# Performance work log

Measured on AMD Instinct MI355X. Metric: run time of the kernel, lower is better.

The kernel has to match this reference:

```python
import jax, jax.numpy as jnp
import numpy as np

EPS_BN = 1e-5
EPS_LN = 1e-5
B_, CIN, COUT, H_, W_ = 8, 64, 128, 64, 64
DSTATE, DCONV, EXPAND = 16, 4, 2
DINNER = EXPAND * COUT            # 256
DTRANK = (COUT + 15) // 16        # 8


def setup_inputs() -> dict:
    key = jax.random.key(0)
    ks = jax.random.split(key, 24)
    g = lambda i, shape, s=0.02: jax.random.normal(ks[i], shape, jnp.float32) * s
    inp = {}
    inp["x"] = jax.random.normal(ks[0], (B_, CIN, H_, W_), jnp.float32)
    # conv-bn-relu x2
    inp["conv1_w"] = g(1, (COUT, CIN, 3, 3), 0.05)
    inp["conv1_b"] = jnp.zeros((COUT,), jnp.float32)
    inp["bn1_g"] = jnp.ones((COUT,), jnp.float32)
    inp["bn1_b"] = jnp.zeros((COUT,), jnp.float32)
    inp["bn1_m"] = g(2, (COUT,), 0.1)
    inp["bn1_v"] = jnp.ones((COUT,), jnp.float32)
    inp["conv2_w"] = g(3, (COUT, COUT, 3, 3), 0.05)
    inp["conv2_b"] = jnp.zeros((COUT,), jnp.float32)
    inp["bn2_g"] = jnp.ones((COUT,), jnp.float32)
    inp["bn2_b"] = jnp.zeros((COUT,), jnp.float32)
    inp["bn2_m"] = g(4, (COUT,), 0.1)
    inp["bn2_v"] = jnp.ones((COUT,), jnp.float32)
    # Mamba params (mamba_ssm defaults: projections bias-free except dt_proj)
    inp["in_proj_w"] = g(5, (2 * DINNER, COUT))
    inp["conv1d_w"] = g(6, (DINNER, 1, DCONV), 0.1)   # depthwise
    inp["conv1d_b"] = jnp.zeros((DINNER,), jnp.float32)
    inp["x_proj_w"] = g(7, (DTRANK + 2 * DSTATE, DINNER))
    inp["dt_proj_w"] = g(8, (DINNER, DTRANK), 0.1)
    inp["dt_proj_b"] = g(9, (DINNER,), 0.5)
    # S4D-real init: A = -[1..d_state] per channel
    A = jnp.tile(jnp.arange(1, DSTATE + 1, dtype=jnp.float32)[None, :], (DINNER, 1))
    inp["A_log"] = jnp.log(A)
    inp["D"] = jnp.ones((DINNER,), jnp.float32)
    inp["out_proj_w"] = g(10, (COUT, DINNER))
    inp["ln_g"] = jnp.ones((COUT,), jnp.float32)
    inp["ln_b"] = jnp.zeros((COUT,), jnp.float32)
    return inp


def _conv3x3(x, w, b):
    y = jax.lax.conv_general_dilated(x, w, (1, 1), ((1, 1), (1, 1)),
                                     dimension_numbers=("NCHW", "OIHW", "NCHW"))
    return y + b[None, :, None, None]


def _bn_eval(x, g, b, m, v):
    inv = jax.lax.rsqrt(v + EPS_BN)
    return (x - m[None, :, None, None]) * (g * inv)[None, :, None, None] + b[None, :, None, None]


def _mamba(x_flat, in_proj_w, conv1d_w, conv1d_b, x_proj_w, dt_proj_w, dt_proj_b, A_log, D, out_proj_w):
    # x_flat: (B, L, C)
    Bsz, L, _ = x_flat.shape
    xz = jnp.einsum("blc,ec->ble", x_flat, in_proj_w)          # (B, L, 2*di)
    xm, z = jnp.split(xz, 2, axis=-1)                           # each (B, L, di)
    # causal depthwise conv1d over time
    xt = jnp.transpose(xm, (0, 2, 1))                           # (B, di, L)
    xt = jax.lax.conv_general_dilated(xt, conv1d_w, (1,), ((DCONV - 1, 0),),
                                      dimension_numbers=("NCH", "OIH", "NCH"),
                                      feature_group_count=DINNER)
    xt = xt + conv1d_b[None, :, None]
    x_ssm = jax.nn.silu(jnp.transpose(xt, (0, 2, 1)))           # (B, L, di)
    xdb = jnp.einsum("bld,ed->ble", x_ssm, x_proj_w)            # (B, L, dt_rank+2*ds)
    dt_r = xdb[..., :DTRANK]
    Bm = xdb[..., DTRANK:DTRANK + DSTATE]                       # (B, L, ds)
    Cm = xdb[..., DTRANK + DSTATE:]                             # (B, L, ds)
    dt = jax.nn.softplus(jnp.einsum("blr,dr->bld", dt_r, dt_proj_w) + dt_proj_b)
    A = -jnp.exp(A_log)                                         # (di, ds)

    def step(h, inp):
        dt_t, B_t, C_t, x_t = inp                               # (B,di) (B,ds) (B,ds) (B,di)
        dA = jnp.exp(dt_t[:, :, None] * A)                      # (B, di, ds)
        h = dA * h + (dt_t * x_t)[:, :, None] * B_t[:, None, :]
        y = jnp.einsum("bds,bs->bd", h, C_t)
        return h, y

    xs = (jnp.swapaxes(dt, 0, 1), jnp.swapaxes(Bm, 0, 1),
          jnp.swapaxes(Cm, 0, 1), jnp.swapaxes(x_ssm, 0, 1))
    h0 = jnp.zeros((Bsz, DINNER, DSTATE), jnp.float32)
    _, ys = jax.lax.scan(step, h0, xs)                          # (L, B, di)
    y = jnp.swapaxes(ys, 0, 1) + D * x_ssm
    y = y * jax.nn.silu(z)
    return jnp.einsum("bld,od->blo", y, out_proj_w)             # (B, L, C)


def reference(x, conv1_w, conv1_b, bn1_g, bn1_b, bn1_m, bn1_v,
              conv2_w, conv2_b, bn2_g, bn2_b, bn2_m, bn2_v,
              in_proj_w, conv1d_w, conv1d_b, x_proj_w, dt_proj_w, dt_proj_b,
              A_log, D, out_proj_w, ln_g, ln_b):
    h = jax.nn.relu(_bn_eval(_conv3x3(x, conv1_w, conv1_b), bn1_g, bn1_b, bn1_m, bn1_v))
    h = jax.nn.relu(_bn_eval(_conv3x3(h, conv2_w, conv2_b), bn2_g, bn2_b, bn2_m, bn2_v))
    Bsz, C, Hh, Ww = h.shape
    seq = jnp.transpose(h, (0, 2, 3, 1)).reshape(Bsz, Hh * Ww, C)
    seq = _mamba(seq, in_proj_w, conv1d_w, conv1d_b, x_proj_w,
                 dt_proj_w, dt_proj_b, A_log, D, out_proj_w)
    # LayerNorm over channels
    mu = jnp.mean(seq, axis=-1, keepdims=True)
    var = jnp.mean(jnp.square(seq - mu), axis=-1, keepdims=True)
    seq = (seq - mu) * jax.lax.rsqrt(var + EPS_LN) * ln_g + ln_b
    return jnp.transpose(seq.reshape(Bsz, Hh, Ww, C), (0, 3, 1, 2))
```

## Files before the change

kernel.cpp:

```cpp
#include <hip/hip_runtime.h>
#include <hip/hip_bf16.h>


typedef __attribute__((ext_vector_type(8))) short bf16x8;
typedef __attribute__((ext_vector_type(4))) float f32x4;

#define DEV __device__ __forceinline__

constexpr float LOG2E = 1.44269504088896f;

DEV float siluf(float v) {
  return v * __builtin_amdgcn_rcpf(1.f + __expf(-v));
}

DEV unsigned short f2bf(float f) {
  __hip_bfloat16 h = __float2bfloat16(f);
  return *reinterpret_cast<unsigned short*>(&h);
}

DEV float bf2f(unsigned short u) {
  unsigned int x = (unsigned int)u << 16;
  return __builtin_bit_cast(float, x);
}

DEV void gll16(const void* g, void* l) {
  __builtin_amdgcn_global_load_lds(
      (const __attribute__((address_space(1))) void*)g,
      (__attribute__((address_space(3))) void*)l, 16, 0, 0);
}

constexpr int NC = 256;
constexpr int CL = 16;

DEV void zero_border(unsigned short* buf, int CI, int tid0, int nthreads) {
  for (int w = tid0; w < 8 * 260; w += nthreads) {
    int b = w / 260, e = w % 260;
    int y, x;
    if (e < 132) { y = (e < 66) ? 0 : 65; x = (e < 66) ? e : e - 66; }
    else { int e2 = e - 132; y = 1 + (e2 >> 1); x = (e2 & 1) ? 65 : 0; }
    uint4* p = reinterpret_cast<uint4*>(buf + ((size_t)((b * 66 + y) * 66 + x)) * CI);
    for (int k = 0; k < CI / 8; ++k) p[k] = uint4{0u, 0u, 0u, 0u};
  }
}

__global__ __launch_bounds__(256) void prologue(
    const float* __restrict__ X, unsigned short* __restrict__ Xb,
    const float* __restrict__ conv1_w, const float* __restrict__ conv2_w,
    const float* __restrict__ in_proj_w, const float* __restrict__ out_proj_w,
    const float* __restrict__ x_proj_w, const float* __restrict__ A_log,
    unsigned short* __restrict__ wb1, unsigned short* __restrict__ wb2,
    unsigned short* __restrict__ win, unsigned short* __restrict__ wout,
    unsigned short* __restrict__ xpwb, float* __restrict__ An2f,
    unsigned short* __restrict__ h1p)
{
  __shared__ float t[64][65];
  const int blk = blockIdx.x;
  const int tid = threadIdx.x;
  if (blk < 512) {
    const int b = blk >> 6, y = blk & 63;
    for (int i = tid; i < 4096; i += 256) {
      int c = i >> 6, xx = i & 63;
      t[c][xx] = X[(((size_t)b * 64 + c) * 64 + y) * 64 + xx];
    }
    __syncthreads();
    for (int i = tid; i < 4096; i += 256) {
      int xx = i >> 6, c = i & 63;
      Xb[(((size_t)(b * 66 + y + 1) * 66) + xx + 1) * 64 + c] = f2bf(t[c][xx]);
    }
  } else if (blk < 1904) {
    int idx = (blk - 512) * 256 + tid;
    if (idx < 73728) {
      int co = idx / 576, r = idx % 576, tp = r >> 6, ci = r & 63;
      wb1[idx] = f2bf(conv1_w[((size_t)co * 64 + ci) * 9 + tp]);
    } else if (idx < 221184) {
      int i = idx - 73728;
      int co = i / 1152, r = i % 1152, tp = r >> 7, ci = r & 127;
      wb2[i] = f2bf(conv2_w[((size_t)co * 128 + ci) * 9 + tp]);
    } else if (idx < 286720) {
      int i = idx - 221184; win[i] = f2bf(in_proj_w[i]);
    } else if (idx < 319488) {
      int i = idx - 286720; wout[i] = f2bf(out_proj_w[i]);
    } else if (idx < 352256) {
      int i = idx - 319488; int r = i >> 8, c = i & 255;
      xpwb[i] = (r < 40) ? f2bf(x_proj_w[r * 256 + c]) : (unsigned short)0;
    } else if (idx < 356352) {
      int i = idx - 352256;
      An2f[i] = -__expf(A_log[i]) * LOG2E;
    }
  } else {
    int tid0 = (blk - 1904) * 256 + tid;
    zero_border(Xb, 64, tid0, 16 * 256);
    zero_border(h1p, 128, tid0, 16 * 256);
  }
}

template<int CI, int PADOUT>
__global__ __launch_bounds__(256) void conv_mfma(
    const unsigned short* __restrict__ Xp,
    const unsigned short* __restrict__ Wb,
    const float* __restrict__ bc,
    const float* __restrict__ bg, const float* __restrict__ bb,
    const float* __restrict__ bm, const float* __restrict__ bv,
    unsigned short* __restrict__ Y)
{
  constexpr int KC  = 3 * CI / 64;
  constexpr int NCH = 3 * KC;
  __shared__ bf16x8 ldsA[2][512];

  const int lane = threadIdx.x & 63;
  const int wid  = threadIdx.x >> 6;
  const int n0 = wid * 32;
  const int y = blockIdx.x, b = blockIdx.y;
  const int lr = lane & 15, kq = lane >> 4, lk = kq * 8;

  auto stage = [&](int buf, int c) {
    const int dy = c / KC, kc = c - dy * KC;
    const unsigned short* g = Xp
        + (size_t)((b * 66 + y + dy) * 66) * CI
        + (size_t)lane * CI + kc * 64 + wid * 16;
    gll16(g,     &ldsA[buf][(wid * 2) * 64]);
    gll16(g + 8, &ldsA[buf][(wid * 2 + 1) * 64]);
  };

  f32x4 acc[4][2];
  #pragma unroll
  for (int i = 0; i < 4; ++i)
    #pragma unroll
    for (int j = 0; j < 2; ++j) acc[i][j] = f32x4{0.f, 0.f, 0.f, 0.f};

  stage(0, 0);
  __syncthreads();

  #pragma unroll
  for (int c = 0; c < NCH; ++c) {
    if (c + 1 < NCH) stage((c + 1) & 1, c + 1);
    const int dy = c / KC, kc = c - dy * KC;
    bf16x8 bw[2][2];
    #pragma unroll
    for (int t = 0; t < 2; ++t)
      #pragma unroll
      for (int nf = 0; nf < 2; ++nf)
        bw[t][nf] = *reinterpret_cast<const bf16x8*>(
            Wb + (size_t)(n0 + nf * 16 + lr) * (9 * CI)
               + dy * 3 * CI + kc * 64 + t * 32 + lk);
    const bf16x8* Ab = ldsA[c & 1];
    #pragma unroll
    for (int t = 0; t < 2; ++t)
      #pragma unroll
      for (int mf = 0; mf < 4; ++mf) {
        bf16x8 afr = Ab[(t * 4 + kq) * 64 + mf * 16 + lr];
        #pragma unroll
        for (int nf = 0; nf < 2; ++nf)
          acc[mf][nf] = __builtin_amdgcn_mfma_f32_16x16x32_bf16(
              afr, bw[t][nf], acc[mf][nf], 0, 0, 0);
      }
    __syncthreads();
  }

  #pragma unroll
  for (int nf = 0; nf < 2; ++nf) {
    int n = n0 + nf * 16 + lr;
    float aS = bg[n] * rsqrtf(bv[n] + 1e-5f);
    float aB = (bc[n] - bm[n]) * aS + bb[n];
    #pragma unroll
    for (int mf = 0; mf < 4; ++mf)
      #pragma unroll
      for (int i = 0; i < 4; ++i) {
        int m = mf * 16 + kq * 4 + i;
        float v = fmaxf(acc[mf][nf][i] * aS + aB, 0.f);
        if (PADOUT)
          Y[((size_t)(b * 66 + y + 1) * 66 + m + 1) * 128 + n] = f2bf(v);
        else
          Y[((size_t)(b * 4096 + y * 64 + m)) * 128 + n] = f2bf(v);
      }
  }
}

template<int KDIM, int EPI>
__global__ __launch_bounds__(256) void gemm_mfma(
    const unsigned short* __restrict__ A,
    const unsigned short* __restrict__ Wn,
    float* __restrict__ C0,
    unsigned short* __restrict__ Cb0, unsigned short* __restrict__ Cb1)
{
  constexpr int NCH = KDIM / 64;
  __shared__ bf16x8 ldsA[2][512];

  const int lane = threadIdx.x & 63;
  const int wid  = threadIdx.x >> 6;
  const int m0 = blockIdx.x * 64;
  const int n0 = blockIdx.y * 128 + wid * 32;
  const int lr = lane & 15, kq = lane >> 4, lk = kq * 8;

  bf16x8 bw[NCH][2][2];
  #pragma unroll
  for (int c = 0; c < NCH; ++c)
    #pragma unroll
    for (int t = 0; t < 2; ++t)
      #pragma unroll
      for (int nf = 0; nf < 2; ++nf)
        bw[c][t][nf] = *reinterpret_cast<const bf16x8*>(
            Wn + (size_t)(n0 + nf * 16 + lr) * KDIM + c * 64 + t * 32 + lk);

  auto stage = [&](int buf, int c) {
    const unsigned short* g = A + (size_t)(m0 + lane) * KDIM + c * 64 + wid * 16;
    gll16(g,     &ldsA[buf][(wid * 2) * 64]);
    gll16(g + 8, &ldsA[buf][(wid * 2 + 1) * 64]);
  };

  f32x4 acc[4][2];
  #pragma unroll
  for (int i = 0; i < 4; ++i)
    #pragma unroll
    for (int j = 0; j < 2; ++j) acc[i][j] = f32x4{0.f, 0.f, 0.f, 0.f};

  stage(0, 0);
  __syncthreads();

  #pragma unroll
  for (int c = 0; c < NCH; ++c) {
    if (c + 1 < NCH) stage((c + 1) & 1, c + 1);
    const bf16x8* Ab = ldsA[c & 1];
    #pragma unroll
    for (int t = 0; t < 2; ++t)
      #pragma unroll
      for (int mf = 0; mf < 4; ++mf) {
        bf16x8 afr = Ab[(t * 4 + kq) * 64 + mf * 16 + lr];
        #pragma unroll
        for (int nf = 0; nf < 2; ++nf)
          acc[mf][nf] = __builtin_amdgcn_mfma_f32_16x16x32_bf16(
              afr, bw[c][t][nf], acc[mf][nf], 0, 0, 0);
      }
    __syncthreads();
  }

  #pragma unroll
  for (int nf = 0; nf < 2; ++nf) {
    int n = n0 + nf * 16 + lr;
    #pragma unroll
    for (int mf = 0; mf < 4; ++mf)
      #pragma unroll
      for (int i = 0; i < 4; ++i) {
        int m = m0 + mf * 16 + kq * 4 + i;
        float v = acc[mf][nf][i];
        if (EPI == 0) {
          if (n < 256) Cb0[(size_t)m * 256 + n] = f2bf(v);
          else         Cb1[(size_t)m * 256 + (n - 256)] = f2bf(v);
        } else {
          if (n < 40) C0[(size_t)m * 40 + n] = v;
        }
      }
  }
}

__global__ __launch_bounds__(256) void outproj_ln(
    const unsigned short* __restrict__ A,
    const unsigned short* __restrict__ Wn,
    const float* __restrict__ lg, const float* __restrict__ lb,
    float* __restrict__ out)
{
  constexpr int KDIM = 256;
  constexpr int NCH = KDIM / 64;
  __shared__ bf16x8 ldsA[2][512];
  __shared__ float buf[64][129];

  const int lane = threadIdx.x & 63;
  const int wid  = threadIdx.x >> 6;
  const int m0 = blockIdx.x * 64;
  const int n0 = wid * 32;
  const int lr = lane & 15, kq = lane >> 4, lk = kq * 8;

  bf16x8 bw[NCH][2][2];
  #pragma unroll
  for (int c = 0; c < NCH; ++c)
    #pragma unroll
    for (int t = 0; t < 2; ++t)
      #pragma unroll
      for (int nf = 0; nf < 2; ++nf)
        bw[c][t][nf] = *reinterpret_cast<const bf16x8*>(
            Wn + (size_t)(n0 + nf * 16 + lr) * KDIM + c * 64 + t * 32 + lk);

  auto stage = [&](int buf2, int c) {
    const unsigned short* g = A + (size_t)(m0 + lane) * KDIM + c * 64 + wid * 16;
    gll16(g,     &ldsA[buf2][(wid * 2) * 64]);
    gll16(g + 8, &ldsA[buf2][(wid * 2 + 1) * 64]);
  };

  f32x4 acc[4][2];
  #pragma unroll
  for (int i = 0; i < 4; ++i)
    #pragma unroll
    for (int j = 0; j < 2; ++j) acc[i][j] = f32x4{0.f, 0.f, 0.f, 0.f};

  stage(0, 0);
  __syncthreads();

  #pragma unroll
  for (int c = 0; c < NCH; ++c) {
    if (c + 1 < NCH) stage((c + 1) & 1, c + 1);
    const bf16x8* Ab = ldsA[c & 1];
    #pragma unroll
    for (int t = 0; t < 2; ++t)
      #pragma unroll
      for (int mf = 0; mf < 4; ++mf) {
        bf16x8 afr = Ab[(t * 4 + kq) * 64 + mf * 16 + lr];
        #pragma unroll
        for (int nf = 0; nf < 2; ++nf)
          acc[mf][nf] = __builtin_amdgcn_mfma_f32_16x16x32_bf16(
              afr, bw[c][t][nf], acc[mf][nf], 0, 0, 0);
      }
    __syncthreads();
  }

  #pragma unroll
  for (int nf = 0; nf < 2; ++nf) {
    int n = n0 + nf * 16 + lr;
    #pragma unroll
    for (int mf = 0; mf < 4; ++mf)
      #pragma unroll
      for (int i = 0; i < 4; ++i)
        buf[mf * 16 + kq * 4 + i][n] = acc[mf][nf][i];
  }
  __syncthreads();

  const int tid = threadIdx.x;
  const int tt = tid >> 2, q = tid & 3;
  float s = 0.f, sq = 0.f;
  #pragma unroll
  for (int i = 0; i < 32; ++i) {
    float v = buf[tt][q * 32 + i];
    s += v; sq += v * v;
  }
  s  += __shfl_xor(s, 1);  s  += __shfl_xor(s, 2);
  sq += __shfl_xor(sq, 1); sq += __shfl_xor(sq, 2);
  float mu = s * (1.f / 128.f);
  float var = sq * (1.f / 128.f) - mu * mu;
  float rstd = rsqrtf(fmaxf(var, 0.f) + 1e-5f);
  #pragma unroll
  for (int i = 0; i < 32; ++i) {
    int c = q * 32 + i;
    buf[tt][c] = (buf[tt][c] - mu) * rstd * lg[c] + lb[c];
  }
  __syncthreads();

  const int bb = m0 >> 12, l0 = m0 & 4095;
  for (int idx = tid; idx < 64 * 128; idx += 256) {
    int c = idx >> 6, t2 = idx & 63;
    out[((size_t)bb * 128 + c) * 4096 + l0 + t2] = buf[t2][c];
  }
}

__global__ __launch_bounds__(256) void conv1d_silu(
    const unsigned short* __restrict__ xm,
    const float* __restrict__ w,
    const float* __restrict__ bias,
    unsigned short* __restrict__ out)
{
  __shared__ float ws4[4][256];
  __shared__ float bsh[256];
  for (int i = threadIdx.x; i < 1024; i += 256)
    ws4[i >> 8][i & 255] = w[(i & 255) * 4 + (i >> 8)];
  bsh[threadIdx.x] = bias[threadIdx.x];
  __syncthreads();
  const int total = 32768 * 32;
  for (int idx = blockIdx.x * 256 + threadIdx.x; idx < total;
       idx += gridDim.x * 256) {
    int d8 = idx & 31, t = idx >> 5, l = t & 4095;
    int d = d8 * 8;
    float acc[8];
    #pragma unroll
    for (int k = 0; k < 8; ++k) acc[k] = bsh[d + k];
    #pragma unroll
    for (int j = 0; j < 4; ++j) {
      if (l - 3 + j >= 0) {
        uint4 xv = *reinterpret_cast<const uint4*>(
            &xm[(size_t)(t - 3 + j) * 256 + d]);
        const unsigned short* xs = reinterpret_cast<const unsigned short*>(&xv);
        #pragma unroll
        for (int k = 0; k < 8; ++k)
          acc[k] = fmaf(bf2f(xs[k]), ws4[j][d + k], acc[k]);
      }
    }
    unsigned int pk[4];
    #pragma unroll
    for (int k = 0; k < 4; ++k) {
      unsigned short lo = f2bf(siluf(acc[2 * k]));
      unsigned short hi = f2bf(siluf(acc[2 * k + 1]));
      pk[k] = (unsigned int)lo | ((unsigned int)hi << 16);
    }
    *reinterpret_cast<uint4*>(&out[(size_t)t * 256 + d]) =
        *reinterpret_cast<uint4*>(pk);
  }
}

__global__ __launch_bounds__(256) void scan_pass1(
    const unsigned short* __restrict__ xssm, const float* __restrict__ xdb,
    const float* __restrict__ dtw, const float* __restrict__ dtb,
    const float* __restrict__ An2f,
    unsigned short* __restrict__ Qb, float* __restrict__ S)
{
  __shared__ __align__(16) float sh[CL][40];
  const int c = blockIdx.x, b = blockIdx.y;
  const int d = threadIdx.x;
  if (threadIdx.x < CL * 10) {
    const float4* src = reinterpret_cast<const float4*>(
        &xdb[((size_t)b * 4096 + c * CL) * 40]);
    reinterpret_cast<float4*>(&sh[0][0])[threadIdx.x] = src[threadIdx.x];
  }
  float4 w0 = *reinterpret_cast<const float4*>(&dtw[d * 8]);
  float4 w1 = *reinterpret_cast<const float4*>(&dtw[d * 8 + 4]);
  const float bdt = dtb[d];
  float An2[16], h[16];
  {
    const f32x4* a2 = reinterpret_cast<const f32x4*>(&An2f[d * 16]);
    #pragma unroll
    for (int q = 0; q < 4; ++q) {
      f32x4 v = a2[q];
      An2[q * 4 + 0] = v[0]; An2[q * 4 + 1] = v[1];
      An2[q * 4 + 2] = v[2]; An2[q * 4 + 3] = v[3];
    }
  }
  #pragma unroll
  for (int s = 0; s < 16; ++s) h[s] = 0.f;
  __syncthreads();

  float sdt = 0.f;
  const size_t xbase = ((size_t)b * 4096 + (size_t)c * CL) * 256 + d;
  unsigned short xu = xssm[xbase];
  for (int l = 0; l < CL; ++l) {
    unsigned short xun = (l + 1 < CL) ? xssm[xbase + (size_t)(l + 1) * 256]
                                      : (unsigned short)0;
    const float4* row = reinterpret_cast<const float4*>(sh[l]);
    float4 r0 = row[0], r1 = row[1];
    float acc = bdt;
    acc = fmaf(r0.x, w0.x, acc); acc = fmaf(r0.y, w0.y, acc);
    acc = fmaf(r0.z, w0.z, acc); acc = fmaf(r0.w, w0.w, acc);
    acc = fmaf(r1.x, w1.x, acc); acc = fmaf(r1.y, w1.y, acc);
    acc = fmaf(r1.z, w1.z, acc); acc = fmaf(r1.w, w1.w, acc);
    float dt = (acc > 20.f) ? acc : __logf(1.f + __expf(acc));
    sdt += dt;
    float dtx = dt * bf2f(xu);
    #pragma unroll
    for (int q = 0; q < 4; ++q) {
      float4 Bq = row[2 + q];
      float bb4[4] = {Bq.x, Bq.y, Bq.z, Bq.w};
      #pragma unroll
      for (int j = 0; j < 4; ++j) {
        int s = q * 4 + j;
        float dA = __builtin_amdgcn_exp2f(dt * An2[s]);
        h[s] = fmaf(dA, h[s], dtx * bb4[j]);
      }
    }
    xu = xun;
  }
  unsigned int pk[8];
  #pragma unroll
  for (int k = 0; k < 8; ++k)
    pk[k] = (unsigned int)f2bf(h[2 * k]) | ((unsigned int)f2bf(h[2 * k + 1]) << 16);
  uint4* qp = reinterpret_cast<uint4*>(
      &Qb[(((size_t)b * NC + c) * 256 + d) * 16]);
  qp[0] = *reinterpret_cast<uint4*>(pk);
  qp[1] = *reinterpret_cast<uint4*>(pk + 4);
  S[((size_t)b * NC + c) * 256 + d] = sdt;
}

__global__ __launch_bounds__(256) void scan_combine(
    unsigned short* __restrict__ Qb, const float* __restrict__ S,
    const float* __restrict__ An2f)
{
  int g = blockIdx.x * 256 + threadIdx.x;
  int b = g >> 12, d = (g >> 4) & 255, s = g & 15;
  float An2 = An2f[d * 16 + s];
  const size_t qbase = (size_t)b * NC * 4096 + d * 16 + s;
  const size_t sbase = (size_t)b * NC * 256 + d;
  float h = 0.f;
  unsigned short qn = Qb[qbase];
  float sn = S[sbase];
  for (int c = 0; c < NC; ++c) {
    float q = bf2f(qn), sd = sn;
    if (c + 1 < NC) {
      qn = Qb[qbase + (size_t)(c + 1) * 4096];
      sn = S[sbase + (size_t)(c + 1) * 256];
    }
    Qb[qbase + (size_t)c * 4096] = f2bf(h);
    h = fmaf(__builtin_amdgcn_exp2f(An2 * sd), h, q);
  }
}

__global__ __launch_bounds__(256) void scan_pass2(
    const unsigned short* __restrict__ xssm, const float* __restrict__ xdb,
    const unsigned short* __restrict__ zb,
    const float* __restrict__ dtw, const float* __restrict__ dtb,
    const float* __restrict__ An2f, const float* __restrict__ Dp,
    const unsigned short* __restrict__ Hstart, unsigned short* __restrict__ ybf)
{
  __shared__ __align__(16) float sh[CL][40];
  const int c = blockIdx.x, b = blockIdx.y;
  const int d = threadIdx.x;
  if (threadIdx.x < CL * 10) {
    const float4* src = reinterpret_cast<const float4*>(
        &xdb[((size_t)b * 4096 + c * CL) * 40]);
    reinterpret_cast<float4*>(&sh[0][0])[threadIdx.x] = src[threadIdx.x];
  }
  float4 w0 = *reinterpret_cast<const float4*>(&dtw[d * 8]);
  float4 w1 = *reinterpret_cast<const float4*>(&dtw[d * 8 + 4]);
  const float bdt = dtb[d];
  const float Dd = Dp[d];
  float An2[16], h[16];
  {
    const f32x4* a2 = reinterpret_cast<const f32x4*>(&An2f[d * 16]);
    #pragma unroll
    for (int q = 0; q < 4; ++q) {
      f32x4 v = a2[q];
      An2[q * 4 + 0] = v[0]; An2[q * 4 + 1] = v[1];
      An2[q * 4 + 2] = v[2]; An2[q * 4 + 3] = v[3];
    }
  }
  {
    const uint4* hp = reinterpret_cast<const uint4*>(
        &Hstart[(((size_t)b * NC + c) * 256 + d) * 16]);
    uint4 h0 = hp[0], h1 = hp[1];
    const unsigned short* hs = reinterpret_cast<const unsigned short*>(&h0);
    #pragma unroll
    for (int s = 0; s < 8; ++s) h[s] = bf2f(hs[s]);
    const unsigned short* hs2 = reinterpret_cast<const unsigned short*>(&h1);
    #pragma unroll
    for (int s = 0; s < 8; ++s) h[8 + s] = bf2f(hs2[s]);
  }
  __syncthreads();

  const size_t xbase = ((size_t)b * 4096 + (size_t)c * CL) * 256 + d;
  unsigned short xu = xssm[xbase], zu = zb[xbase];
  for (int l = 0; l < CL; ++l) {
    unsigned short xun = 0, zun = 0;
    if (l + 1 < CL) {
      xun = xssm[xbase + (size_t)(l + 1) * 256];
      zun = zb[xbase + (size_t)(l + 1) * 256];
    }
    const float4* row = reinterpret_cast<const float4*>(sh[l]);
    float4 r0 = row[0], r1 = row[1];
    float acc = bdt;
    acc = fmaf(r0.x, w0.x, acc); acc = fmaf(r0.y, w0.y, acc);
    acc = fmaf(r0.z, w0.z, acc); acc = fmaf(r0.w, w0.w, acc);
    acc = fmaf(r1.x, w1.x, acc); acc = fmaf(r1.y, w1.y, acc);
    acc = fmaf(r1.z, w1.z, acc); acc = fmaf(r1.w, w1.w, acc);
    float dt = (acc > 20.f) ? acc : __logf(1.f + __expf(acc));
    float xv = bf2f(xu);
    float dtx = dt * xv;
    float yq[4] = {0.f, 0.f, 0.f, 0.f};
    #pragma unroll
    for (int q = 0; q < 4; ++q) {
      float4 Bq = row[2 + q], Cq = row[6 + q];
      float bb4[4] = {Bq.x, Bq.y, Bq.z, Bq.w};
      float cc4[4] = {Cq.x, Cq.y, Cq.z, Cq.w};
      #pragma unroll
      for (int j = 0; j < 4; ++j) {
        int s = q * 4 + j;
        float dA = __builtin_amdgcn_exp2f(dt * An2[s]);
        h[s] = fmaf(dA, h[s], dtx * bb4[j]);
        yq[q] = fmaf(h[s], cc4[j], yq[q]);
      }
    }
    float y = (yq[0] + yq[1]) + (yq[2] + yq[3]);
    y = (y + Dd * xv) * siluf(bf2f(zu));
    ybf[xbase + (size_t)l * 256] = f2bf(y);
    xu = xun; zu = zun;
  }
}

extern "C" void kernel_launch(void* const* d_in, const int* in_sizes, int n_in,
                              void* d_out, int out_size, void* d_ws, size_t ws_size,
                              hipStream_t stream) {
  const float* x        = (const float*)d_in[0];
  const float* conv1_w  = (const float*)d_in[1];
  const float* conv1_b  = (const float*)d_in[2];
  const float* bn1_g    = (const float*)d_in[3];
  const float* bn1_b    = (const float*)d_in[4];
  const float* bn1_m    = (const float*)d_in[5];
  const float* bn1_v    = (const float*)d_in[6];
  const float* conv2_w  = (const float*)d_in[7];
  const float* conv2_b  = (const float*)d_in[8];
  const float* bn2_g    = (const float*)d_in[9];
  const float* bn2_b    = (const float*)d_in[10];
  const float* bn2_m    = (const float*)d_in[11];
  const float* bn2_v    = (const float*)d_in[12];
  const float* in_proj_w  = (const float*)d_in[13];
  const float* conv1d_w   = (const float*)d_in[14];
  const float* conv1d_b   = (const float*)d_in[15];
  const float* x_proj_w   = (const float*)d_in[16];
  const float* dt_proj_w  = (const float*)d_in[17];
  const float* dt_proj_b  = (const float*)d_in[18];
  const float* A_log      = (const float*)d_in[19];
  const float* Dp         = (const float*)d_in[20];
  const float* out_proj_w = (const float*)d_in[21];
  const float* ln_g       = (const float*)d_in[22];
  const float* ln_b       = (const float*)d_in[23];
  float* out = (float*)d_out;

  float* ws_f = (float*)d_ws;
  unsigned short* xbp  = (unsigned short*)ws_f;
  unsigned short* xmb  = (unsigned short*)ws_f;
  unsigned short* ybf  = (unsigned short*)ws_f;
  float*          xdb  = ws_f + 4194304;
  float*          Sbuf = ws_f + 5505024;
  unsigned short* zbu  = (unsigned short*)(ws_f + 8388608);
  unsigned short* xsu  = (unsigned short*)(ws_f + 12582912);
  unsigned short* h1p  = (unsigned short*)(ws_f + 16777216);
  unsigned short* seqb = (unsigned short*)(ws_f + 19007488);
  unsigned short* Qb   = (unsigned short*)(ws_f + 16777216);
  unsigned short* wb1  = (unsigned short*)(ws_f + 25165824);
  unsigned short* wb2  = (unsigned short*)(ws_f + 25202688);
  unsigned short* win  = (unsigned short*)(ws_f + 25276416);
  unsigned short* wout = (unsigned short*)(ws_f + 25309184);
  unsigned short* xpwb = (unsigned short*)(ws_f + 25325568);
  float*          An2f = ws_f + 25341952;

  prologue<<<1920, 256, 0, stream>>>(
      x, xbp, conv1_w, conv2_w, in_proj_w, out_proj_w, x_proj_w, A_log,
      wb1, wb2, win, wout, xpwb, An2f, h1p);

  conv_mfma<64, 1><<<dim3(64, 8), 256, 0, stream>>>(
      xbp, wb1, conv1_b, bn1_g, bn1_b, bn1_m, bn1_v, h1p);
  conv_mfma<128, 0><<<dim3(64, 8), 256, 0, stream>>>(
      h1p, wb2, conv2_b, bn2_g, bn2_b, bn2_m, bn2_v, seqb);

  gemm_mfma<128, 0><<<dim3(512, 4), 256, 0, stream>>>(
      seqb, win, nullptr, xmb, zbu);

  conv1d_silu<<<2048, 256, 0, stream>>>(xmb, conv1d_w, conv1d_b, xsu);

  gemm_mfma<256, 2><<<dim3(512, 1), 256, 0, stream>>>(
      xsu, xpwb, xdb, nullptr, nullptr);

  scan_pass1<<<dim3(NC, 8), 256, 0, stream>>>(
      xsu, xdb, dt_proj_w, dt_proj_b, An2f, Qb, Sbuf);
  scan_combine<<<128, 256, 0, stream>>>(Qb, Sbuf, An2f);
  scan_pass2<<<dim3(NC, 8), 256, 0, stream>>>(
      xsu, xdb, zbu, dt_proj_w, dt_proj_b, An2f, Dp, Qb, ybf);

  outproj_ln<<<512, 256, 0, stream>>>(ybf, wout, ln_g, ln_b, out);
}
```

Measured before the change: 207.2 us.

## Fuse in_proj with causal conv1d+SiLU and compute x_proj inside scan passes

The in_proj GEMM now applies the depthwise causal conv1d and SiLU in its epilogue through an LDS tile, recomputing the three halo rows from the input and weights. It also applies SiLU to z up front, so the scan no longer does it. The separate conv1d and x_proj kernels are removed, and each scan pass computes the x_proj (dt/B/C) columns for its chunk with MFMA. This cuts two launches and the global round trips for the pre-conv activations and the x_proj output. In exchange, x_proj is computed twice (once per scan pass), the halo rows are recomputed redundantly, and the intermediate values are rounded to bf16 at slightly different points.

```diff
diff --git a/kernel.cpp b/kernel.cpp
--- a/kernel.cpp
+++ b/kernel.cpp
@@ -176,25 +176,46 @@
   }
 }
 
-template<int KDIM, int EPI>
-__global__ __launch_bounds__(256) void gemm_mfma(
+__global__ __launch_bounds__(256) void inproj_fused(
     const unsigned short* __restrict__ A,
     const unsigned short* __restrict__ Wn,
-    float* __restrict__ C0,
-    unsigned short* __restrict__ Cb0, unsigned short* __restrict__ Cb1)
+    const float* __restrict__ c1w,
+    const float* __restrict__ c1b,
+    unsigned short* __restrict__ xsu,
+    unsigned short* __restrict__ zbu)
 {
-  constexpr int NCH = KDIM / 64;
+  constexpr int KDIM = 128;
   __shared__ bf16x8 ldsA[2][512];
-
-  const int lane = threadIdx.x & 63;
-  const int wid  = threadIdx.x >> 6;
+  __shared__ unsigned short xmt[67][136];
+  __shared__ unsigned short s3[3][128];
+  __shared__ float cw[128][4];
+  __shared__ float cbias[128];
+
+  const int tid = threadIdx.x;
+  const int lane = tid & 63, wid = tid >> 6;
   const int m0 = blockIdx.x * 64;
-  const int n0 = blockIdx.y * 128 + wid * 32;
+  const int by = blockIdx.y;
+  const int n0 = by * 128 + wid * 32;
   const int lr = lane & 15, kq = lane >> 4, lk = kq * 8;
-
-  bf16x8 bw[NCH][2][2];
-  #pragma unroll
-  for (int c = 0; c < NCH; ++c)
+  const int l0 = m0 & 4095;
+
+  if (by < 2) {
+    for (int w = tid; w < 384; w += 256) {
+      int j = w >> 7, k = w & 127;
+      s3[j][k] = (l0 == 0) ? (unsigned short)0
+                           : A[(size_t)(m0 - 3 + j) * 128 + k];
+    }
+    if (tid < 128) {
+      int dd = by * 128 + tid;
+      cw[tid][0] = c1w[dd * 4 + 0]; cw[tid][1] = c1w[dd * 4 + 1];
+      cw[tid][2] = c1w[dd * 4 + 2]; cw[tid][3] = c1w[dd * 4 + 3];
+      cbias[tid] = c1b[dd];
+    }
+  }
+
+  bf16x8 bw[2][2][2];
+  #pragma unroll
+  for (int c = 0; c < 2; ++c)
     #pragma unroll
     for (int t = 0; t < 2; ++t)
       #pragma unroll
@@ -218,8 +239,8 @@
   __syncthreads();
 
   #pragma unroll
-  for (int c = 0; c < NCH; ++c) {
-    if (c + 1 < NCH) stage((c + 1) & 1, c + 1);
+  for (int c = 0; c < 2; ++c) {
+    if (c + 1 < 2) stage((c + 1) & 1, c + 1);
     const bf16x8* Ab = ldsA[c & 1];
     #pragma unroll
     for (int t = 0; t < 2; ++t)
@@ -234,22 +255,81 @@
     __syncthreads();
   }
 
+  if (by >= 2) {
+    #pragma unroll
+    for (int nf = 0; nf < 2; ++nf) {
+      int n = n0 + nf * 16 + lr - 256;
+      #pragma unroll
+      for (int mf = 0; mf < 4; ++mf)
+        #pragma unroll
+        for (int i = 0; i < 4; ++i)
+          zbu[(size_t)(m0 + mf * 16 + kq * 4 + i) * 256 + n] =
+              f2bf(siluf(acc[mf][nf][i]));
+    }
+    return;
+  }
+
   #pragma unroll
   for (int nf = 0; nf < 2; ++nf) {
-    int n = n0 + nf * 16 + lr;
+    int ch = wid * 32 + nf * 16 + lr;
     #pragma unroll
     for (int mf = 0; mf < 4; ++mf)
       #pragma unroll
-      for (int i = 0; i < 4; ++i) {
-        int m = m0 + mf * 16 + kq * 4 + i;
-        float v = acc[mf][nf][i];
-        if (EPI == 0) {
-          if (n < 256) Cb0[(size_t)m * 256 + n] = f2bf(v);
-          else         Cb1[(size_t)m * 256 + (n - 256)] = f2bf(v);
-        } else {
-          if (n < 40) C0[(size_t)m * 40 + n] = v;
-        }
+      for (int i = 0; i < 4; ++i)
+        xmt[3 + mf * 16 + kq * 4 + i][ch] = f2bf(acc[mf][nf][i]);
+  }
+  __syncthreads();
+
+  for (int w = tid; w < 384; w += 256) {
+    int j = w >> 7, ch = w & 127;
+    float a = 0.f;
+    if (l0 != 0) {
+      const unsigned short* wr = Wn + (size_t)(by * 128 + ch) * 128;
+      #pragma unroll 4
+      for (int k0 = 0; k0 < 128; k0 += 8) {
+        bf16x8 wv = *reinterpret_cast<const bf16x8*>(wr + k0);
+        #pragma unroll
+        for (int k = 0; k < 8; ++k)
+          a = fmaf(bf2f(s3[j][k0 + k]), bf2f((unsigned short)wv[k]), a);
       }
+    }
+    xmt[j][ch] = f2bf(a);
+  }
+  __syncthreads();
+
+  const int tg = tid & 15, ch8 = tid >> 4;
+  float wr8[8][4], br8[8];
+  #pragma unroll
+  for (int k = 0; k < 8; ++k) {
+    int chl = ch8 * 8 + k;
+    wr8[k][0] = cw[chl][0]; wr8[k][1] = cw[chl][1];
+    wr8[k][2] = cw[chl][2]; wr8[k][3] = cw[chl][3];
+    br8[k] = cbias[chl];
+  }
+  #pragma unroll
+  for (int tk = 0; tk < 4; ++tk) {
+    int m = tg * 4 + tk;
+    float o[8];
+    #pragma unroll
+    for (int k = 0; k < 8; ++k) o[k] = br8[k];
+    #pragma unroll
+    for (int j = 0; j < 4; ++j) {
+      uint4 xv = *reinterpret_cast<const uint4*>(&xmt[m + j][ch8 * 8]);
+      const unsigned short* xs = reinterpret_cast<const unsigned short*>(&xv);
+      #pragma unroll
+      for (int k = 0; k < 8; ++k)
+        o[k] = fmaf(bf2f(xs[k]), wr8[k][j], o[k]);
+    }
+    unsigned int pk[4];
+    #pragma unroll
+    for (int k = 0; k < 4; ++k) {
+      unsigned short lo = f2bf(siluf(o[2 * k]));
+      unsigned short hi = f2bf(siluf(o[2 * k + 1]));
+      pk[k] = (unsigned int)lo | ((unsigned int)hi << 16);
+    }
+    *reinterpret_cast<uint4*>(
+        &xsu[(size_t)(m0 + m) * 256 + by * 128 + ch8 * 8]) =
+        *reinterpret_cast<uint4*>(pk);
   }
 }
 
@@ -350,51 +430,9 @@
   }
 }
 
-__global__ __launch_bounds__(256) void conv1d_silu(
-    const unsigned short* __restrict__ xm,
-    const float* __restrict__ w,
-    const float* __restrict__ bias,
-    unsigned short* __restrict__ out)
-{
-  __shared__ float ws4[4][256];
-  __shared__ float bsh[256];
-  for (int i = threadIdx.x; i < 1024; i += 256)
-    ws4[i >> 8][i & 255] = w[(i & 255) * 4 + (i >> 8)];
-  bsh[threadIdx.x] = bias[threadIdx.x];
-  __syncthreads();
-  const int total = 32768 * 32;
-  for (int idx = blockIdx.x * 256 + threadIdx.x; idx < total;
-       idx += gridDim.x * 256) {
-    int d8 = idx & 31, t = idx >> 5, l = t & 4095;
-    int d = d8 * 8;
-    float acc[8];
-    #pragma unroll
-    for (int k = 0; k < 8; ++k) acc[k] = bsh[d + k];
-    #pragma unroll
-    for (int j = 0; j < 4; ++j) {
-      if (l - 3 + j >= 0) {
-        uint4 xv = *reinterpret_cast<const uint4*>(
-            &xm[(size_t)(t - 3 + j) * 256 + d]);
-        const unsigned short* xs = reinterpret_cast<const unsigned short*>(&xv);
-        #pragma unroll
-        for (int k = 0; k < 8; ++k)
-          acc[k] = fmaf(bf2f(xs[k]), ws4[j][d + k], acc[k]);
-      }
-    }
-    unsigned int pk[4];
-    #pragma unroll
-    for (int k = 0; k < 4; ++k) {
-      unsigned short lo = f2bf(siluf(acc[2 * k]));
-      unsigned short hi = f2bf(siluf(acc[2 * k + 1]));
-      pk[k] = (unsigned int)lo | ((unsigned int)hi << 16);
-    }
-    *reinterpret_cast<uint4*>(&out[(size_t)t * 256 + d]) =
-        *reinterpret_cast<uint4*>(pk);
-  }
-}
-
 __global__ __launch_bounds__(256) void scan_pass1(
-    const unsigned short* __restrict__ xssm, const float* __restrict__ xdb,
+    const unsigned short* __restrict__ xssm,
+    const unsigned short* __restrict__ xpw,
     const float* __restrict__ dtw, const float* __restrict__ dtb,
     const float* __restrict__ An2f,
     unsigned short* __restrict__ Qb, float* __restrict__ S)
@@ -402,10 +440,26 @@
   __shared__ __align__(16) float sh[CL][40];
   const int c = blockIdx.x, b = blockIdx.y;
   const int d = threadIdx.x;
-  if (threadIdx.x < CL * 10) {
-    const float4* src = reinterpret_cast<const float4*>(
-        &xdb[((size_t)b * 4096 + c * CL) * 40]);
-    reinterpret_cast<float4*>(&sh[0][0])[threadIdx.x] = src[threadIdx.x];
+  const int lane = threadIdx.x & 63, wid = threadIdx.x >> 6;
+  if (wid < 3) {
+    const int col0 = wid * 16;
+    const int plr = lane & 15, plk = (lane >> 4) * 8;
+    f32x4 pacc = f32x4{0.f, 0.f, 0.f, 0.f};
+    const unsigned short* Xrow =
+        xssm + ((size_t)b * 4096 + (size_t)c * CL + plr) * 256;
+    const unsigned short* Wrow = xpw + (size_t)(col0 + plr) * 256;
+    #pragma unroll
+    for (int k0 = 0; k0 < 256; k0 += 32) {
+      bf16x8 af = *reinterpret_cast<const bf16x8*>(Xrow + k0 + plk);
+      bf16x8 bf = *reinterpret_cast<const bf16x8*>(Wrow + k0 + plk);
+      pacc = __builtin_amdgcn_mfma_f32_16x16x32_bf16(af, bf, pacc, 0, 0, 0);
+    }
+    int col = col0 + (lane & 15);
+    if (col < 40) {
+      #pragma unroll
+      for (int i = 0; i < 4; ++i)
+        sh[(lane >> 4) * 4 + i][col] = pacc[i];
+    }
   }
   float4 w0 = *reinterpret_cast<const float4*>(&dtw[d * 8]);
   float4 w1 = *reinterpret_cast<const float4*>(&dtw[d * 8 + 4]);
@@ -488,7 +542,8 @@
 }
 
 __global__ __launch_bounds__(256) void scan_pass2(
-    const unsigned short* __restrict__ xssm, const float* __restrict__ xdb,
+    const unsigned short* __restrict__ xssm,
+    const unsigned short* __restrict__ xpw,
     const unsigned short* __restrict__ zb,
     const float* __restrict__ dtw, const float* __restrict__ dtb,
     const float* __restrict__ An2f, const float* __restrict__ Dp,
@@ -497,10 +552,26 @@
   __shared__ __align__(16) float sh[CL][40];
   const int c = blockIdx.x, b = blockIdx.y;
   const int d = threadIdx.x;
-  if (threadIdx.x < CL * 10) {
-    const float4* src = reinterpret_cast<const float4*>(
-        &xdb[((size_t)b * 4096 + c * CL) * 40]);
-    reinterpret_cast<float4*>(&sh[0][0])[threadIdx.x] = src[threadIdx.x];
+  const int lane = threadIdx.x & 63, wid = threadIdx.x >> 6;
+  if (wid < 3) {
+    const int col0 = wid * 16;
+    const int plr = lane & 15, plk = (lane >> 4) * 8;
+    f32x4 pacc = f32x4{0.f, 0.f, 0.f, 0.f};
+    const unsigned short* Xrow =
+        xssm + ((size_t)b * 4096 + (size_t)c * CL + plr) * 256;
+    const unsigned short* Wrow = xpw + (size_t)(col0 + plr) * 256;
+    #pragma unroll
+    for (int k0 = 0; k0 < 256; k0 += 32) {
+      bf16x8 af = *reinterpret_cast<const bf16x8*>(Xrow + k0 + plk);
+      bf16x8 bf = *reinterpret_cast<const bf16x8*>(Wrow + k0 + plk);
+      pacc = __builtin_amdgcn_mfma_f32_16x16x32_bf16(af, bf, pacc, 0, 0, 0);
+    }
+    int col = col0 + (lane & 15);
+    if (col < 40) {
+      #pragma unroll
+      for (int i = 0; i < 4; ++i)
+        sh[(lane >> 4) * 4 + i][col] = pacc[i];
+    }
   }
   float4 w0 = *reinterpret_cast<const float4*>(&dtw[d * 8]);
   float4 w1 = *reinterpret_cast<const float4*>(&dtw[d * 8 + 4]);
@@ -562,7 +633,7 @@
       }
     }
     float y = (yq[0] + yq[1]) + (yq[2] + yq[3]);
-    y = (y + Dd * xv) * siluf(bf2f(zu));
+    y = (y + Dd * xv) * bf2f(zu);
     ybf[xbase + (size_t)l * 256] = f2bf(y);
     xu = xun; zu = zun;
   }
@@ -599,9 +670,7 @@
 
   float* ws_f = (float*)d_ws;
   unsigned short* xbp  = (unsigned short*)ws_f;
-  unsigned short* xmb  = (unsigned short*)ws_f;
   unsigned short* ybf  = (unsigned short*)ws_f;
-  float*          xdb  = ws_f + 4194304;
   float*          Sbuf = ws_f + 5505024;
   unsigned short* zbu  = (unsigned short*)(ws_f + 8388608);
   unsigned short* xsu  = (unsigned short*)(ws_f + 12582912);
@@ -624,19 +693,14 @@
   conv_mfma<128, 0><<<dim3(64, 8), 256, 0, stream>>>(
       h1p, wb2, conv2_b, bn2_g, bn2_b, bn2_m, bn2_v, seqb);
 
-  gemm_mfma<128, 0><<<dim3(512, 4), 256, 0, stream>>>(
-      seqb, win, nullptr, xmb, zbu);
-
-  conv1d_silu<<<2048, 256, 0, stream>>>(xmb, conv1d_w, conv1d_b, xsu);
-
-  gemm_mfma<256, 2><<<dim3(512, 1), 256, 0, stream>>>(
-      xsu, xpwb, xdb, nullptr, nullptr);
+  inproj_fused<<<dim3(512, 4), 256, 0, stream>>>(
+      seqb, win, conv1d_w, conv1d_b, xsu, zbu);
 
   scan_pass1<<<dim3(NC, 8), 256, 0, stream>>>(
-      xsu, xdb, dt_proj_w, dt_proj_b, An2f, Qb, Sbuf);
+      xsu, xpwb, dt_proj_w, dt_proj_b, An2f, Qb, Sbuf);
   scan_combine<<<128, 256, 0, stream>>>(Qb, Sbuf, An2f);
   scan_pass2<<<dim3(NC, 8), 256, 0, stream>>>(
-      xsu, xdb, zbu, dt_proj_w, dt_proj_b, An2f, Dp, Qb, ybf);
+      xsu, xpwb, zbu, dt_proj_w, dt_proj_b, An2f, Dp, Qb, ybf);
 
   outproj_ln<<<512, 256, 0, stream>>>(ybf, wout, ln_g, ln_b, out);
 }
```

Measured after the change: 212.6 us. +2.6%, slower.
